# Kernel tuning notes

Measured on AMD Instinct MI355X. Metric: run time of the kernel, lower is better.

The kernel has to match this reference:

```python
import jax, jax.numpy as jnp
import numpy as np

EPS = 1e-05


def setup_inputs() -> dict:
    key = jax.random.key(0)
    k1, k2, k3 = jax.random.split(key, 3)
    b, s, n, m = 16, 4096, 1024, 1024
    x = jax.random.normal(k1, (b, s, n), dtype=jnp.float32)
    # torch.rand -> uniform [0,1)
    A = jax.random.uniform(k2, (m, n), dtype=jnp.float32)
    B = jax.random.uniform(k3, (m, n), dtype=jnp.float32)
    return {"x": x, "A": A, "B": B}


def reference(x, A, B):
    # query: project each token with A, then sum over seq -> [b, m]
    query = jnp.einsum('ij,bsj->bi', A, x)  # fused projection + seq-sum
    query = query / (EPS + jnp.linalg.norm(query, axis=1, keepdims=True))
    # keys: [b, s, m], L2-normalized per token
    keys = jnp.einsum('ij,bsj->bsi', B, x)
    keys = keys / (EPS + jnp.linalg.norm(keys, axis=2, keepdims=True))
    # cosine-style similarity (no softmax): [b, s]
    sim = jnp.einsum('bi,bsi->bs', query, keys)
    # weighted sum of raw inputs: [b, n]
    out = jnp.einsum('bs,bsn->bn', sim, x)
    return (out, sim)
```

## Files before the change

kernel.cpp:

```cpp
#include <hip/hip_runtime.h>

#define EPS 1e-5f

typedef __bf16 bf16x8 __attribute__((ext_vector_type(8)));
typedef __bf16 bf16x4 __attribute__((ext_vector_type(4)));
typedef float f32x4 __attribute__((ext_vector_type(4)));

static __device__ __forceinline__ unsigned int f2bf(float f) {
    unsigned int u = __builtin_bit_cast(unsigned int, f);
    u = (u + 0x7fffu + ((u >> 16) & 1u)) >> 16;
    return u;
}

static __device__ __forceinline__ void gll16(const void* g, void* l) {
    __builtin_amdgcn_global_load_lds(
        (const __attribute__((address_space(1))) unsigned int*)(unsigned long long)g,
        (__attribute__((address_space(3))) unsigned int*)(unsigned int)(unsigned long long)l,
        16, 0, 0);
}

template <int XBF>
__global__ __launch_bounds__(256) void k_prep(const float* __restrict__ x,
                                              float* __restrict__ xs_part,
                                              unsigned short* __restrict__ xbf) {
    const int b = blockIdx.y, sc = blockIdx.x, tid = threadIdx.x;
    const size_t rowbase = ((size_t)(b * 4096 + sc * 128)) * 1024;
    const float4* src = (const float4*)(x + rowbase) + tid;
    uint2* dst = XBF ? ((uint2*)(xbf + rowbase) + tid) : (uint2*)0;
    float ax = 0.f, ay = 0.f, az = 0.f, aw = 0.f;
    for (int r = 0; r < 128; ++r) {
        float4 v = src[r * 256];
        ax += v.x; ay += v.y; az += v.z; aw += v.w;
        if (XBF) {
            uint2 p;
            p.x = f2bf(v.x) | (f2bf(v.y) << 16);
            p.y = f2bf(v.z) | (f2bf(v.w) << 16);
            dst[r * 256] = p;
        }
    }
    float4 o; o.x = ax; o.y = ay; o.z = az; o.w = aw;
    ((float4*)(xs_part + ((size_t)(b * 32 + sc)) * 1024))[tid] = o;
}

__global__ void k_xsred(const float* __restrict__ xs_part, float* __restrict__ xs) {
    const int b = blockIdx.y, j = blockIdx.x * 256 + threadIdx.x;
    const float* p = xs_part + (size_t)b * 32 * 1024 + j;
    float s = 0.f;
#pragma unroll
    for (int sc = 0; sc < 32; ++sc) s += p[sc * 1024];
    xs[b * 1024 + j] = s;
}

__global__ void k_bconv(const float* __restrict__ B, unsigned short* __restrict__ Bb) {
    const int i = blockIdx.x * 256 + threadIdx.x;
    float4 v = ((const float4*)B)[i];
    uint2 p;
    p.x = f2bf(v.x) | (f2bf(v.y) << 16);
    p.y = f2bf(v.z) | (f2bf(v.w) << 16);
    ((uint2*)Bb)[i] = p;
}

__global__ void k_query(const float* __restrict__ A, const float* __restrict__ xs,
                        float* __restrict__ q) {
    const int b = blockIdx.y;
    const int i = blockIdx.x * 256 + threadIdx.x;
    const float4* ar = (const float4*)(A + (size_t)i * 1024);
    const float4* xr = (const float4*)(xs + b * 1024);
    float acc = 0.f;
    for (int k = 0; k < 256; ++k) {
        float4 a = ar[k], v = xr[k];
        acc += a.x * v.x + a.y * v.y + a.z * v.z + a.w * v.w;
    }
    q[b * 1024 + i] = acc;
}

__global__ void k_qnorm(float* q) {
    const int b = blockIdx.x, tid = threadIdx.x;
    float4* qp = (float4*)(q + (size_t)b * 1024);
    float4 v = qp[tid];
    float ss = v.x * v.x + v.y * v.y + v.z * v.z + v.w * v.w;
    for (int o = 1; o < 64; o <<= 1) ss += __shfl_xor(ss, o);
    __shared__ float wsum[4];
    if ((tid & 63) == 0) wsum[tid >> 6] = ss;
    __syncthreads();
    float inv = 1.f / (EPS + sqrtf(wsum[0] + wsum[1] + wsum[2] + wsum[3]));
    v.x *= inv; v.y *= inv; v.z *= inv; v.w *= inv;
    qp[tid] = v;
}

__global__ void k_w(const float* __restrict__ B, const float* __restrict__ q,
                    float* __restrict__ w) {
    const int b = blockIdx.y;
    const int j = blockIdx.x * 256 + threadIdx.x;
    const float* qb = q + (size_t)b * 1024;
    float acc = 0.f;
    for (int i = 0; i < 1024; ++i) acc += B[(size_t)i * 1024 + j] * qb[i];
    w[b * 1024 + j] = acc;
}

__global__ __launch_bounds__(512, 2) void k_nsq8(const unsigned short* __restrict__ xbf,
                                                 const unsigned short* __restrict__ Bb,
                                                 float* __restrict__ nsq_g) {
    __shared__ __align__(16) unsigned short Xs[2][256 * 64];
    __shared__ __align__(16) unsigned short Bs[2][256 * 64];
    __shared__ float nsq_s[256];

    const int tid = threadIdx.x;
    const int lane = tid & 63;
    const int l15 = lane & 15, lg = lane >> 4;
    const int w = tid >> 6;
    const int wm = w >> 2, wn = w & 3;
    const size_t tok0 = (size_t)blockIdx.x * 256;

#define STAGE(s_, buf_)                                                                  \
    do {                                                                                 \
        const int mt_ = (s_) >> 4, ks_ = (s_) & 15;                                      \
        _Pragma("unroll") for (int it = 0; it < 4; ++it) {                               \
            const int g_ = it * 512 + tid;                                               \
            const int row_ = g_ >> 3, c_ = g_ & 7;                                       \
            const int csw_ = (c_ ^ (row_ & 7)) * 8;                                      \
            char* bx_ = (char*)Xs[buf_] + (size_t)(it * 512 + (tid & ~63)) * 16;         \
            gll16(xbf + (tok0 + row_) * 1024 + ks_ * 64 + csw_, bx_);                    \
            char* bb_ = (char*)Bs[buf_] + (size_t)(it * 512 + (tid & ~63)) * 16;         \
            gll16(Bb + (size_t)(mt_ * 256 + row_) * 1024 + ks_ * 64 + csw_, bb_);        \
        }                                                                                \
    } while (0)

    float nsq_reg[8][4];
#pragma unroll
    for (int mi = 0; mi < 8; ++mi)
#pragma unroll
        for (int r = 0; r < 4; ++r) nsq_reg[mi][r] = 0.f;

    f32x4 acc[8][4];

    STAGE(0, 0);
    STAGE(1, 1);

    for (int s = 0; s < 64; ++s) {
        const int buf = s & 1;
        if ((s & 15) == 0) {
#pragma unroll
            for (int mi = 0; mi < 8; ++mi)
#pragma unroll
                for (int ni = 0; ni < 4; ++ni) acc[mi][ni] = (f32x4){0.f, 0.f, 0.f, 0.f};
        }
        if (s < 62) asm volatile("s_waitcnt vmcnt(8)" ::: "memory");
        else        asm volatile("s_waitcnt vmcnt(0)" ::: "memory");
        __builtin_amdgcn_s_barrier();

        const char* xb = (const char*)Xs[buf] + (wm * 128 + l15) * 128;
        const char* bb = (const char*)Bs[buf] + (wn * 64 + l15) * 128;
        const int sw = (l15 & 7) << 4;

        bf16x8 bq[4][2];
#pragma unroll
        for (int ni = 0; ni < 4; ++ni)
#pragma unroll
            for (int kk = 0; kk < 2; ++kk)
                bq[ni][kk] = *(const bf16x8*)(bb + ni * 16 * 128 + ((kk * 64 + lg * 16) ^ sw));

        __builtin_amdgcn_s_setprio(1);
#pragma unroll
        for (int p = 0; p < 4; ++p) {
            bf16x8 a[2][2];
#pragma unroll
            for (int mi = 0; mi < 2; ++mi)
#pragma unroll
                for (int kk = 0; kk < 2; ++kk)
                    a[mi][kk] = *(const bf16x8*)(xb + (p * 2 + mi) * 16 * 128 +
                                                 ((kk * 64 + lg * 16) ^ sw));
#pragma unroll
            for (int mi = 0; mi < 2; ++mi)
#pragma unroll
                for (int ni = 0; ni < 4; ++ni)
#pragma unroll
                    for (int kk = 0; kk < 2; ++kk)
                        acc[p * 2 + mi][ni] = __builtin_amdgcn_mfma_f32_16x16x32_bf16(
                            a[mi][kk], bq[ni][kk], acc[p * 2 + mi][ni], 0, 0, 0);
        }
        __builtin_amdgcn_s_setprio(0);

        asm volatile("" ::: "memory");
        __builtin_amdgcn_s_barrier();
        asm volatile("" ::: "memory");
        if (s + 2 < 64) STAGE(s + 2, buf);

        if ((s & 15) == 15) {
#pragma unroll
            for (int mi = 0; mi < 8; ++mi)
#pragma unroll
                for (int ni = 0; ni < 4; ++ni)
#pragma unroll
                    for (int r = 0; r < 4; ++r)
                        nsq_reg[mi][r] += acc[mi][ni][r] * acc[mi][ni][r];
        }
    }
#undef STAGE

    if (tid < 256) nsq_s[tid] = 0.f;
    __syncthreads();
#pragma unroll
    for (int mi = 0; mi < 8; ++mi)
#pragma unroll
        for (int r = 0; r < 4; ++r) {
            float v = nsq_reg[mi][r];
            v += __shfl_xor(v, 1);
            v += __shfl_xor(v, 2);
            v += __shfl_xor(v, 4);
            v += __shfl_xor(v, 8);
            if (l15 == 0) atomicAdd(&nsq_s[wm * 128 + mi * 16 + lg * 4 + r], v);
        }
    __syncthreads();
    if (tid < 256) nsq_g[tok0 + tid] = nsq_s[tid];
}

__global__ __launch_bounds__(256, 2) void k_nsq_f32(const float* __restrict__ x,
                                                    const unsigned short* __restrict__ Bb,
                                                    float* __restrict__ nsq_g) {
    __shared__ unsigned short Xs[128 * 64];
    __shared__ unsigned short Bs[128 * 64];
    __shared__ float nsq_s[128];

    const int tid = threadIdx.x;
    const int lane = tid & 63;
    const int l15 = lane & 15, lg = lane >> 4;
    const int w = tid >> 6;
    const int wr = w >> 1, wc = w & 1;
    const int st = blockIdx.x * 128;
    const int mh = blockIdx.y;

    float nsq_reg[4][4];
#pragma unroll
    for (int mi = 0; mi < 4; ++mi)
#pragma unroll
        for (int r = 0; r < 4; ++r) nsq_reg[mi][r] = 0.f;

    for (int mti = 0; mti < 4; ++mti) {
        const int mt = mh * 4 + mti;
        f32x4 acc[4][4];
#pragma unroll
        for (int mi = 0; mi < 4; ++mi)
#pragma unroll
            for (int ni = 0; ni < 4; ++ni) acc[mi][ni] = (f32x4){0.f, 0.f, 0.f, 0.f};

        for (int ks = 0; ks < 16; ++ks) {
            __syncthreads();
            {
                const int row = tid >> 1, kh = tid & 1;
                const float* srcx = x + (size_t)(st + row) * 1024 + ks * 64 + kh * 32;
                char* ldsrow = (char*)Xs + row * 128;
                const int sw = (row & 7) << 4;
#pragma unroll
                for (int j = 0; j < 4; ++j) {
                    float4 v0 = ((const float4*)srcx)[j * 2];
                    float4 v1 = ((const float4*)srcx)[j * 2 + 1];
                    uint4 p;
                    p.x = f2bf(v0.x) | (f2bf(v0.y) << 16);
                    p.y = f2bf(v0.z) | (f2bf(v0.w) << 16);
                    p.z = f2bf(v1.x) | (f2bf(v1.y) << 16);
                    p.w = f2bf(v1.z) | (f2bf(v1.w) << 16);
                    *(uint4*)(ldsrow + (((kh * 4 + j) * 16) ^ sw)) = p;
                }
#pragma unroll
                for (int it = 0; it < 4; ++it) {
                    const int idx = it * 256 + tid;
                    const int brow = idx >> 3, c = idx & 7;
                    char* baseB = (char*)Bs + (size_t)(it * 256 + (tid & ~63)) * 16;
                    gll16(Bb + (size_t)(mt * 128 + brow) * 1024 + ks * 64 + (c ^ (brow & 7)) * 8,
                          baseB);
                }
            }
            __syncthreads();

            const char* xb = (const char*)Xs + (wr * 64 + l15) * 128;
            const char* bb = (const char*)Bs + (wc * 64 + l15) * 128;
            const int sw = (l15 & 7) << 4;
#pragma unroll
            for (int kk = 0; kk < 2; ++kk) {
                const int ob = (kk * 64 + lg * 16) ^ sw;
                bf16x8 a[4], bq[4];
#pragma unroll
                for (int mi = 0; mi < 4; ++mi) a[mi] = *(const bf16x8*)(xb + mi * 2048 + ob);
#pragma unroll
                for (int ni = 0; ni < 4; ++ni) bq[ni] = *(const bf16x8*)(bb + ni * 2048 + ob);
#pragma unroll
                for (int mi = 0; mi < 4; ++mi)
#pragma unroll
                    for (int ni = 0; ni < 4; ++ni)
                        acc[mi][ni] = __builtin_amdgcn_mfma_f32_16x16x32_bf16(
                            a[mi], bq[ni], acc[mi][ni], 0, 0, 0);
            }
        }
#pragma unroll
        for (int mi = 0; mi < 4; ++mi)
#pragma unroll
            for (int ni = 0; ni < 4; ++ni)
#pragma unroll
                for (int r = 0; r < 4; ++r)
                    nsq_reg[mi][r] += acc[mi][ni][r] * acc[mi][ni][r];
    }

    if (tid < 128) nsq_s[tid] = 0.f;
    __syncthreads();
#pragma unroll
    for (int mi = 0; mi < 4; ++mi)
#pragma unroll
        for (int r = 0; r < 4; ++r) {
            float v = nsq_reg[mi][r];
            v += __shfl_xor(v, 1);
            v += __shfl_xor(v, 2);
            v += __shfl_xor(v, 4);
            v += __shfl_xor(v, 8);
            if (l15 == 0) atomicAdd(&nsq_s[wr * 64 + mi * 16 + lg * 4 + r], v);
        }
    __syncthreads();
    if (tid < 128) nsq_g[(size_t)mh * 65536 + st + tid] = nsq_s[tid];
}

template <int XBF>
__global__ __launch_bounds__(256, 2) void k_finish(
    const float* __restrict__ x, const unsigned short* __restrict__ xbf,
    const float* __restrict__ w, const float* __restrict__ nsq_g,
    float* __restrict__ outp, float* __restrict__ sim_out) {
    __shared__ __align__(16) unsigned short xt[32 * 1024];
    __shared__ float numer[32];
    __shared__ float simv[32];

    const int tid = threadIdx.x;
    const int bs = blockIdx.x;
    const int b = bs >> 7, s0 = (bs & 127) * 32;
    const size_t tok0 = (size_t)b * 4096 + s0;

    if (XBF) {
#pragma unroll
        for (int it = 0; it < 16; ++it) {
            const int idx = it * 256 + tid;
            const int row = idx >> 7, c = idx & 127;
            char* base = (char*)xt + (size_t)(it * 256 + (tid & ~63)) * 16;
            gll16(xbf + (tok0 + row) * 1024 + ((c ^ (row & 7)) * 8), base);
        }
    } else {
        const float4* src = (const float4*)(x + tok0 * 1024) + tid;
        char* lds = (char*)xt;
        for (int r = 0; r < 32; ++r) {
            float4 v = src[r * 256];
            uint2 p;
            p.x = f2bf(v.x) | (f2bf(v.y) << 16);
            p.y = f2bf(v.z) | (f2bf(v.w) << 16);
            *(uint2*)(lds + r * 2048 + ((tid * 8) ^ ((r & 7) << 4))) = p;
        }
    }
    __syncthreads();

    {
        const int t = tid >> 3, kp = tid & 7;
        const float* wb = w + (size_t)b * 1024 + kp * 128;
        const char* pt = (const char*)xt + t * 2048;
        const int sw2 = (t & 7) << 4;
        float acc = 0.f;
#pragma unroll
        for (int j = 0; j < 16; ++j) {
            const int kb = (kp * 128 + j * 8) * 2;
            bf16x8 v = *(const bf16x8*)(pt + (kb ^ sw2));
#pragma unroll
            for (int e = 0; e < 8; ++e) acc += (float)v[e] * wb[j * 8 + e];
        }
        acc += __shfl_xor(acc, 1);
        acc += __shfl_xor(acc, 2);
        acc += __shfl_xor(acc, 4);
        if (kp == 0) numer[t] = acc;
    }
    __syncthreads();

    if (tid < 32) {
        float nt = XBF ? nsq_g[tok0 + tid] : (nsq_g[tok0 + tid] + nsq_g[65536 + tok0 + tid]);
        float s = numer[tid] / (EPS + sqrtf(nt));
        simv[tid] = s;
        sim_out[tok0 + tid] = s;
    }
    __syncthreads();

    {
        const int n0 = tid * 4;
        float a0 = 0.f, a1 = 0.f, a2 = 0.f, a3 = 0.f;
        const char* lds = (const char*)xt;
#pragma unroll 4
        for (int t = 0; t < 32; ++t) {
            int byte = t * 2048 + ((n0 * 2) ^ ((t & 7) << 4));
            bf16x4 v = *(const bf16x4*)(lds + byte);
            float s = simv[t];
            a0 += s * (float)v[0];
            a1 += s * (float)v[1];
            a2 += s * (float)v[2];
            a3 += s * (float)v[3];
        }
        float4 o; o.x = a0; o.y = a1; o.z = a2; o.w = a3;
        ((float4*)(outp + (size_t)bs * 1024))[tid] = o;
    }
}

__global__ void k_outred(const float* __restrict__ outp, float* __restrict__ out) {
    const int b = blockIdx.y, j = blockIdx.x * 256 + threadIdx.x;
    const float* p = outp + (size_t)b * 128 * 1024 + j;
    float s = 0.f;
    for (int t = 0; t < 128; ++t) s += p[t * 1024];
    out[b * 1024 + j] = s;
}

extern "C" void kernel_launch(void* const* d_in, const int* in_sizes, int n_in,
                              void* d_out, int out_size, void* d_ws, size_t ws_size,
                              hipStream_t stream) {
    const float* x = (const float*)d_in[0];
    const float* A = (const float*)d_in[1];
    const float* B = (const float*)d_in[2];
    float* out = (float*)d_out;
    float* sim = out + 16 * 1024;
    float* ws = (float*)d_ws;
    float* xs_part = ws;
    float* xs = ws + 524288;
    float* q = ws + 540672;
    float* wv = ws + 557056;
    float* nsq = ws + 573440;
    float* outp = ws + 704512;
    unsigned short* Bb = (unsigned short*)(ws + 2801664);
    unsigned short* xbf = (unsigned short*)(ws + 3325952);
    const bool xb = ws_size >= (size_t)(3325952 + 33554432) * 4;

    if (xb) k_prep<1><<<dim3(32, 16), 256, 0, stream>>>(x, xs_part, xbf);
    else    k_prep<0><<<dim3(32, 16), 256, 0, stream>>>(x, xs_part, (unsigned short*)0);
    k_bconv<<<1024, 256, 0, stream>>>(B, Bb);
    k_xsred<<<dim3(4, 16), 256, 0, stream>>>(xs_part, xs);
    k_query<<<dim3(4, 16), 256, 0, stream>>>(A, xs, q);
    k_qnorm<<<16, 256, 0, stream>>>(q);
    k_w<<<dim3(4, 16), 256, 0, stream>>>(B, q, wv);
    if (xb) k_nsq8<<<256, 512, 0, stream>>>(xbf, Bb, nsq);
    else    k_nsq_f32<<<dim3(512, 2), 256, 0, stream>>>(x, Bb, nsq);
    if (xb) k_finish<1><<<2048, 256, 0, stream>>>(x, xbf, wv, nsq, outp, sim);
    else    k_finish<0><<<2048, 256, 0, stream>>>(x, xbf, wv, nsq, outp, sim);
    k_outred<<<dim3(4, 16), 256, 0, stream>>>(outp, out);
}
```

Measured before the change: 324.8 us.

## Fuse finish stage into GEMM kernel and merge small query/norm kernels

Merges the xs reduction into the query kernel and the q normalization into the w kernel, which removes launches. The bf16 key-norm GEMM kernel now also computes sim and the partial weighted sums for its 256 tokens. It reloads x tiles into the reused LDS union, so the separate finish kernel and the nsq round-trip through global memory go away. The GEMM prefetch is split into smaller pieces interleaved across the MFMA sub-steps, with a barrier after each, and the norm reduction is done per m-tile using LDS atomics. In exchange it adds more barriers and runs the finish phase serially at low parallelism (256 blocks), which may leave the GPU underused.

```diff
diff --git a/kernel.cpp b/kernel.cpp
--- a/kernel.cpp
+++ b/kernel.cpp
@@ -4,6 +4,7 @@
 
 typedef __bf16 bf16x8 __attribute__((ext_vector_type(8)));
 typedef __bf16 bf16x4 __attribute__((ext_vector_type(4)));
+typedef __bf16 bf16x2 __attribute__((ext_vector_type(2)));
 typedef float f32x4 __attribute__((ext_vector_type(4)));
 
 static __device__ __forceinline__ unsigned int f2bf(float f) {
@@ -42,15 +43,6 @@
     ((float4*)(xs_part + ((size_t)(b * 32 + sc)) * 1024))[tid] = o;
 }
 
-__global__ void k_xsred(const float* __restrict__ xs_part, float* __restrict__ xs) {
-    const int b = blockIdx.y, j = blockIdx.x * 256 + threadIdx.x;
-    const float* p = xs_part + (size_t)b * 32 * 1024 + j;
-    float s = 0.f;
-#pragma unroll
-    for (int sc = 0; sc < 32; ++sc) s += p[sc * 1024];
-    xs[b * 1024 + j] = s;
-}
-
 __global__ void k_bconv(const float* __restrict__ B, unsigned short* __restrict__ Bb) {
     const int i = blockIdx.x * 256 + threadIdx.x;
     float4 v = ((const float4*)B)[i];
@@ -60,82 +52,107 @@
     ((uint2*)Bb)[i] = p;
 }
 
-__global__ void k_query(const float* __restrict__ A, const float* __restrict__ xs,
-                        float* __restrict__ q) {
-    const int b = blockIdx.y;
-    const int i = blockIdx.x * 256 + threadIdx.x;
+__global__ __launch_bounds__(256) void k_queryf(const float* __restrict__ xs_part,
+                                                const float* __restrict__ A,
+                                                float* __restrict__ q) {
+    __shared__ float xsl[1024];
+    const int b = blockIdx.y, g = blockIdx.x, tid = threadIdx.x;
+    {
+        float4 s4 = {0.f, 0.f, 0.f, 0.f};
+        const float4* p = (const float4*)(xs_part + (size_t)b * 32768) + tid;
+        for (int sc = 0; sc < 32; ++sc) {
+            float4 v = p[sc * 256];
+            s4.x += v.x; s4.y += v.y; s4.z += v.z; s4.w += v.w;
+        }
+        ((float4*)xsl)[tid] = s4;
+    }
+    __syncthreads();
+    const int i = g * 256 + tid;
     const float4* ar = (const float4*)(A + (size_t)i * 1024);
-    const float4* xr = (const float4*)(xs + b * 1024);
     float acc = 0.f;
     for (int k = 0; k < 256; ++k) {
-        float4 a = ar[k], v = xr[k];
+        float4 a = ar[k], v = ((const float4*)xsl)[k];
         acc += a.x * v.x + a.y * v.y + a.z * v.z + a.w * v.w;
     }
     q[b * 1024 + i] = acc;
 }
 
-__global__ void k_qnorm(float* q) {
-    const int b = blockIdx.x, tid = threadIdx.x;
-    float4* qp = (float4*)(q + (size_t)b * 1024);
-    float4 v = qp[tid];
+__global__ __launch_bounds__(256) void k_wf(const float* __restrict__ B,
+                                            const float* __restrict__ q,
+                                            float* __restrict__ w) {
+    __shared__ float ql[1024];
+    __shared__ float wsum[4];
+    const int b = blockIdx.y, g = blockIdx.x, tid = threadIdx.x;
+    float4 v = ((const float4*)(q + (size_t)b * 1024))[tid];
     float ss = v.x * v.x + v.y * v.y + v.z * v.z + v.w * v.w;
     for (int o = 1; o < 64; o <<= 1) ss += __shfl_xor(ss, o);
-    __shared__ float wsum[4];
     if ((tid & 63) == 0) wsum[tid >> 6] = ss;
     __syncthreads();
-    float inv = 1.f / (EPS + sqrtf(wsum[0] + wsum[1] + wsum[2] + wsum[3]));
-    v.x *= inv; v.y *= inv; v.z *= inv; v.w *= inv;
-    qp[tid] = v;
-}
-
-__global__ void k_w(const float* __restrict__ B, const float* __restrict__ q,
-                    float* __restrict__ w) {
-    const int b = blockIdx.y;
-    const int j = blockIdx.x * 256 + threadIdx.x;
-    const float* qb = q + (size_t)b * 1024;
+    const float inv = 1.f / (EPS + sqrtf(wsum[0] + wsum[1] + wsum[2] + wsum[3]));
+    float4 n; n.x = v.x * inv; n.y = v.y * inv; n.z = v.z * inv; n.w = v.w * inv;
+    ((float4*)ql)[tid] = n;
+    __syncthreads();
+    const int j = g * 256 + tid;
     float acc = 0.f;
-    for (int i = 0; i < 1024; ++i) acc += B[(size_t)i * 1024 + j] * qb[i];
+    for (int i = 0; i < 1024; ++i) acc += B[(size_t)i * 1024 + j] * ql[i];
     w[b * 1024 + j] = acc;
 }
 
-__global__ __launch_bounds__(512, 2) void k_nsq8(const unsigned short* __restrict__ xbf,
-                                                 const unsigned short* __restrict__ Bb,
-                                                 float* __restrict__ nsq_g) {
-    __shared__ __align__(16) unsigned short Xs[2][256 * 64];
-    __shared__ __align__(16) unsigned short Bs[2][256 * 64];
+__global__ __launch_bounds__(512, 2) void k_main2(const unsigned short* __restrict__ xbf,
+                                                  const unsigned short* __restrict__ Bb,
+                                                  const float* __restrict__ w,
+                                                  float* __restrict__ outp,
+                                                  float* __restrict__ sim_out) {
+    __shared__ __align__(16) union {
+        struct { unsigned short Xs[2][256 * 64]; unsigned short Bs[2][256 * 64]; } g;
+        unsigned short xt[32 * 1024];
+    } S;
     __shared__ float nsq_s[256];
+    __shared__ float wlds[1024];
+    __shared__ float numer_s[32];
+    __shared__ float simv[32];
 
     const int tid = threadIdx.x;
     const int lane = tid & 63;
     const int l15 = lane & 15, lg = lane >> 4;
-    const int w = tid >> 6;
-    const int wm = w >> 2, wn = w & 3;
-    const size_t tok0 = (size_t)blockIdx.x * 256;
-
-#define STAGE(s_, buf_)                                                                  \
-    do {                                                                                 \
-        const int mt_ = (s_) >> 4, ks_ = (s_) & 15;                                      \
-        _Pragma("unroll") for (int it = 0; it < 4; ++it) {                               \
-            const int g_ = it * 512 + tid;                                               \
-            const int row_ = g_ >> 3, c_ = g_ & 7;                                       \
-            const int csw_ = (c_ ^ (row_ & 7)) * 8;                                      \
-            char* bx_ = (char*)Xs[buf_] + (size_t)(it * 512 + (tid & ~63)) * 16;         \
-            gll16(xbf + (tok0 + row_) * 1024 + ks_ * 64 + csw_, bx_);                    \
-            char* bb_ = (char*)Bs[buf_] + (size_t)(it * 512 + (tid & ~63)) * 16;         \
-            gll16(Bb + (size_t)(mt_ * 256 + row_) * 1024 + ks_ * 64 + csw_, bb_);        \
-        }                                                                                \
+    const int w8 = tid >> 6;
+    const int wm = w8 >> 2, wn = w8 & 3;
+    const int bx = blockIdx.x;
+    const size_t tok0 = (size_t)bx * 256;
+    const int b = bx >> 4;
+
+    ((float2*)wlds)[tid] = ((const float2*)(w + (size_t)b * 1024))[tid];
+    if (tid < 256) nsq_s[tid] = 0.f;
+
+#define STAGE_B(ts_, bf_, it_)                                                            \
+    do {                                                                                  \
+        const int mt_ = (ts_) >> 4, ks_ = (ts_) & 15;                                     \
+        const int g_ = (it_) * 512 + tid;                                                 \
+        const int row_ = g_ >> 3, c_ = g_ & 7;                                            \
+        gll16(Bb + (size_t)(mt_ * 256 + row_) * 1024 + ks_ * 64 + ((c_ ^ (row_ & 7)) * 8),\
+              (char*)S.g.Bs[bf_] + (size_t)((it_) * 512 + (tid & ~63)) * 16);             \
     } while (0)
-
-    float nsq_reg[8][4];
-#pragma unroll
-    for (int mi = 0; mi < 8; ++mi)
-#pragma unroll
-        for (int r = 0; r < 4; ++r) nsq_reg[mi][r] = 0.f;
+#define STAGE_X(ts_, bf_, p_)                                                             \
+    do {                                                                                  \
+        const int ks_ = (ts_) & 15;                                                       \
+        const int w_ = tid >> 6;                                                          \
+        const int ar0_ = (w_ < 4) ? ((p_) * 32 + w_ * 8) : (128 + (p_) * 32 + (w_ - 4) * 8); \
+        const int ar_ = ar0_ + ((tid & 63) >> 3);                                         \
+        const int c_ = tid & 7;                                                           \
+        gll16(xbf + (tok0 + ar_) * 1024 + ks_ * 64 + ((c_ ^ (ar_ & 7)) * 8),              \
+              (char*)S.g.Xs[bf_] + (size_t)ar0_ * 128);                                   \
+    } while (0)
 
     f32x4 acc[8][4];
 
-    STAGE(0, 0);
-    STAGE(1, 1);
+#pragma unroll
+    for (int it = 0; it < 4; ++it) STAGE_B(0, 0, it);
+#pragma unroll
+    for (int pp = 0; pp < 4; ++pp) STAGE_X(0, 0, pp);
+#pragma unroll
+    for (int it = 0; it < 4; ++it) STAGE_B(1, 1, it);
+#pragma unroll
+    for (int pp = 0; pp < 4; ++pp) STAGE_X(1, 1, pp);
 
     for (int s = 0; s < 64; ++s) {
         const int buf = s & 1;
@@ -149,9 +166,10 @@
         else        asm volatile("s_waitcnt vmcnt(0)" ::: "memory");
         __builtin_amdgcn_s_barrier();
 
-        const char* xb = (const char*)Xs[buf] + (wm * 128 + l15) * 128;
-        const char* bb = (const char*)Bs[buf] + (wn * 64 + l15) * 128;
+        const char* xb = (const char*)S.g.Xs[buf] + (wm * 128 + l15) * 128;
+        const char* bb = (const char*)S.g.Bs[buf] + (wn * 64 + l15) * 128;
         const int sw = (l15 & 7) << 4;
+        const bool pre = (s + 2 < 64);
 
         bf16x8 bq[4][2];
 #pragma unroll
@@ -160,7 +178,6 @@
             for (int kk = 0; kk < 2; ++kk)
                 bq[ni][kk] = *(const bf16x8*)(bb + ni * 16 * 128 + ((kk * 64 + lg * 16) ^ sw));
 
-        __builtin_amdgcn_s_setprio(1);
 #pragma unroll
         for (int p = 0; p < 4; ++p) {
             bf16x8 a[2][2];
@@ -170,6 +187,14 @@
                 for (int kk = 0; kk < 2; ++kk)
                     a[mi][kk] = *(const bf16x8*)(xb + (p * 2 + mi) * 16 * 128 +
                                                  ((kk * 64 + lg * 16) ^ sw));
+            if (pre) {
+                if (p == 1) { STAGE_B(s + 2, buf, 0); STAGE_B(s + 2, buf, 1); STAGE_X(s + 2, buf, 0); }
+                if (p == 2) { STAGE_B(s + 2, buf, 2); STAGE_B(s + 2, buf, 3); STAGE_X(s + 2, buf, 1); }
+                if (p == 3) { STAGE_X(s + 2, buf, 2); }
+            }
+            asm volatile("" ::: "memory");
+            __builtin_amdgcn_s_barrier();
+            __builtin_amdgcn_s_setprio(1);
 #pragma unroll
             for (int mi = 0; mi < 2; ++mi)
 #pragma unroll
@@ -178,41 +203,83 @@
                     for (int kk = 0; kk < 2; ++kk)
                         acc[p * 2 + mi][ni] = __builtin_amdgcn_mfma_f32_16x16x32_bf16(
                             a[mi][kk], bq[ni][kk], acc[p * 2 + mi][ni], 0, 0, 0);
-        }
-        __builtin_amdgcn_s_setprio(0);
-
-        asm volatile("" ::: "memory");
-        __builtin_amdgcn_s_barrier();
-        asm volatile("" ::: "memory");
-        if (s + 2 < 64) STAGE(s + 2, buf);
+            __builtin_amdgcn_s_setprio(0);
+            asm volatile("" ::: "memory");
+            __builtin_amdgcn_s_barrier();
+        }
+        if (pre) STAGE_X(s + 2, buf, 3);
 
         if ((s & 15) == 15) {
 #pragma unroll
             for (int mi = 0; mi < 8; ++mi)
 #pragma unroll
-                for (int ni = 0; ni < 4; ++ni)
-#pragma unroll
-                    for (int r = 0; r < 4; ++r)
-                        nsq_reg[mi][r] += acc[mi][ni][r] * acc[mi][ni][r];
-        }
-    }
-#undef STAGE
-
-    if (tid < 256) nsq_s[tid] = 0.f;
-    __syncthreads();
-#pragma unroll
-    for (int mi = 0; mi < 8; ++mi)
-#pragma unroll
-        for (int r = 0; r < 4; ++r) {
-            float v = nsq_reg[mi][r];
-            v += __shfl_xor(v, 1);
-            v += __shfl_xor(v, 2);
-            v += __shfl_xor(v, 4);
-            v += __shfl_xor(v, 8);
-            if (l15 == 0) atomicAdd(&nsq_s[wm * 128 + mi * 16 + lg * 4 + r], v);
-        }
-    __syncthreads();
-    if (tid < 256) nsq_g[tok0 + tid] = nsq_s[tid];
+                for (int r = 0; r < 4; ++r) {
+                    float v = 0.f;
+#pragma unroll
+                    for (int ni = 0; ni < 4; ++ni) v += acc[mi][ni][r] * acc[mi][ni][r];
+                    v += __shfl_xor(v, 1);
+                    v += __shfl_xor(v, 2);
+                    v += __shfl_xor(v, 4);
+                    v += __shfl_xor(v, 8);
+                    if (l15 == 0) atomicAdd(&nsq_s[wm * 128 + mi * 16 + lg * 4 + r], v);
+                }
+        }
+    }
+#undef STAGE_B
+#undef STAGE_X
+    __syncthreads();
+
+    float oa0 = 0.f, oa1 = 0.f;
+    for (int sub = 0; sub < 8; ++sub) {
+#pragma unroll
+        for (int it = 0; it < 8; ++it) {
+            const int idx = it * 512 + tid;
+            const int row = idx >> 7, c = idx & 127;
+            gll16(xbf + (tok0 + sub * 32 + row) * 1024 + (c ^ (row & 7)) * 8,
+                  (char*)S.xt + (size_t)(it * 512 + (tid & ~63)) * 16);
+        }
+        asm volatile("s_waitcnt vmcnt(0)" ::: "memory");
+        __syncthreads();
+        {
+            const int t = tid >> 4, kp = tid & 15;
+            const char* pt = (const char*)S.xt + t * 2048;
+            const int sw2 = (t & 7) << 4;
+            float acc2 = 0.f;
+#pragma unroll
+            for (int j = 0; j < 8; ++j) {
+                bf16x8 v = *(const bf16x8*)(pt + ((j * 256 + kp * 16) ^ sw2));
+                const float* wp = wlds + j * 128 + kp * 8;
+#pragma unroll
+                for (int e = 0; e < 8; ++e) acc2 += (float)v[e] * wp[e];
+            }
+            acc2 += __shfl_xor(acc2, 1);
+            acc2 += __shfl_xor(acc2, 2);
+            acc2 += __shfl_xor(acc2, 4);
+            acc2 += __shfl_xor(acc2, 8);
+            if (kp == 0) numer_s[t] = acc2;
+        }
+        __syncthreads();
+        if (tid < 32) {
+            float sv = numer_s[tid] / (EPS + sqrtf(nsq_s[sub * 32 + tid]));
+            simv[tid] = sv;
+            sim_out[tok0 + sub * 32 + tid] = sv;
+        }
+        __syncthreads();
+        {
+            const char* lds = (const char*)S.xt;
+            const int nb = tid * 4;
+#pragma unroll 4
+            for (int t = 0; t < 32; ++t) {
+                bf16x2 v = *(const bf16x2*)(lds + t * 2048 + (nb ^ ((t & 7) << 4)));
+                float sv = simv[t];
+                oa0 += sv * (float)v[0];
+                oa1 += sv * (float)v[1];
+            }
+        }
+        __syncthreads();
+    }
+    float2 o; o.x = oa0; o.y = oa1;
+    ((float2*)(outp + (size_t)bx * 1024))[tid] = o;
 }
 
 __global__ __launch_bounds__(256, 2) void k_nsq_f32(const float* __restrict__ x,
@@ -318,11 +385,10 @@
     if (tid < 128) nsq_g[(size_t)mh * 65536 + st + tid] = nsq_s[tid];
 }
 
-template <int XBF>
-__global__ __launch_bounds__(256, 2) void k_finish(
-    const float* __restrict__ x, const unsigned short* __restrict__ xbf,
-    const float* __restrict__ w, const float* __restrict__ nsq_g,
-    float* __restrict__ outp, float* __restrict__ sim_out) {
+__global__ __launch_bounds__(256, 2) void k_finish0(
+    const float* __restrict__ x, const float* __restrict__ w,
+    const float* __restrict__ nsq_g, float* __restrict__ outp,
+    float* __restrict__ sim_out) {
     __shared__ __align__(16) unsigned short xt[32 * 1024];
     __shared__ float numer[32];
     __shared__ float simv[32];
@@ -332,24 +398,14 @@
     const int b = bs >> 7, s0 = (bs & 127) * 32;
     const size_t tok0 = (size_t)b * 4096 + s0;
 
-    if (XBF) {
-#pragma unroll
-        for (int it = 0; it < 16; ++it) {
-            const int idx = it * 256 + tid;
-            const int row = idx >> 7, c = idx & 127;
-            char* base = (char*)xt + (size_t)(it * 256 + (tid & ~63)) * 16;
-            gll16(xbf + (tok0 + row) * 1024 + ((c ^ (row & 7)) * 8), base);
-        }
-    } else {
-        const float4* src = (const float4*)(x + tok0 * 1024) + tid;
-        char* lds = (char*)xt;
-        for (int r = 0; r < 32; ++r) {
-            float4 v = src[r * 256];
-            uint2 p;
-            p.x = f2bf(v.x) | (f2bf(v.y) << 16);
-            p.y = f2bf(v.z) | (f2bf(v.w) << 16);
-            *(uint2*)(lds + r * 2048 + ((tid * 8) ^ ((r & 7) << 4))) = p;
-        }
+    const float4* src = (const float4*)(x + tok0 * 1024) + tid;
+    char* lds = (char*)xt;
+    for (int r = 0; r < 32; ++r) {
+        float4 v = src[r * 256];
+        uint2 p;
+        p.x = f2bf(v.x) | (f2bf(v.y) << 16);
+        p.y = f2bf(v.z) | (f2bf(v.w) << 16);
+        *(uint2*)(lds + r * 2048 + ((tid * 8) ^ ((r & 7) << 4))) = p;
     }
     __syncthreads();
 
@@ -374,7 +430,7 @@
     __syncthreads();
 
     if (tid < 32) {
-        float nt = XBF ? nsq_g[tok0 + tid] : (nsq_g[tok0 + tid] + nsq_g[65536 + tok0 + tid]);
+        float nt = nsq_g[tok0 + tid] + nsq_g[65536 + tok0 + tid];
         float s = numer[tid] / (EPS + sqrtf(nt));
         simv[tid] = s;
         sim_out[tok0 + tid] = s;
@@ -384,11 +440,11 @@
     {
         const int n0 = tid * 4;
         float a0 = 0.f, a1 = 0.f, a2 = 0.f, a3 = 0.f;
-        const char* lds = (const char*)xt;
+        const char* p = (const char*)xt;
 #pragma unroll 4
         for (int t = 0; t < 32; ++t) {
             int byte = t * 2048 + ((n0 * 2) ^ ((t & 7) << 4));
-            bf16x4 v = *(const bf16x4*)(lds + byte);
+            bf16x4 v = *(const bf16x4*)(p + byte);
             float s = simv[t];
             a0 += s * (float)v[0];
             a1 += s * (float)v[1];
@@ -400,11 +456,12 @@
     }
 }
 
+template <int NT>
 __global__ void k_outred(const float* __restrict__ outp, float* __restrict__ out) {
     const int b = blockIdx.y, j = blockIdx.x * 256 + threadIdx.x;
-    const float* p = outp + (size_t)b * 128 * 1024 + j;
+    const float* p = outp + (size_t)b * NT * 1024 + j;
     float s = 0.f;
-    for (int t = 0; t < 128; ++t) s += p[t * 1024];
+    for (int t = 0; t < NT; ++t) s += p[t * 1024];
     out[b * 1024 + j] = s;
 }
 
@@ -418,7 +475,6 @@
     float* sim = out + 16 * 1024;
     float* ws = (float*)d_ws;
     float* xs_part = ws;
-    float* xs = ws + 524288;
     float* q = ws + 540672;
     float* wv = ws + 557056;
     float* nsq = ws + 573440;
@@ -430,13 +486,14 @@
     if (xb) k_prep<1><<<dim3(32, 16), 256, 0, stream>>>(x, xs_part, xbf);
     else    k_prep<0><<<dim3(32, 16), 256, 0, stream>>>(x, xs_part, (unsigned short*)0);
     k_bconv<<<1024, 256, 0, stream>>>(B, Bb);
-    k_xsred<<<dim3(4, 16), 256, 0, stream>>>(xs_part, xs);
-    k_query<<<dim3(4, 16), 256, 0, stream>>>(A, xs, q);
-    k_qnorm<<<16, 256, 0, stream>>>(q);
-    k_w<<<dim3(4, 16), 256, 0, stream>>>(B, q, wv);
-    if (xb) k_nsq8<<<256, 512, 0, stream>>>(xbf, Bb, nsq);
-    else    k_nsq_f32<<<dim3(512, 2), 256, 0, stream>>>(x, Bb, nsq);
-    if (xb) k_finish<1><<<2048, 256, 0, stream>>>(x, xbf, wv, nsq, outp, sim);
-    else    k_finish<0><<<2048, 256, 0, stream>>>(x, xbf, wv, nsq, outp, sim);
-    k_outred<<<dim3(4, 16), 256, 0, stream>>>(outp, out);
-}
+    k_queryf<<<dim3(4, 16), 256, 0, stream>>>(xs_part, A, q);
+    k_wf<<<dim3(4, 16), 256, 0, stream>>>(B, q, wv);
+    if (xb) {
+        k_main2<<<256, 512, 0, stream>>>(xbf, Bb, wv, outp, sim);
+        k_outred<16><<<dim3(4, 16), 256, 0, stream>>>(outp, out);
+    } else {
+        k_nsq_f32<<<dim3(512, 2), 256, 0, stream>>>(x, Bb, nsq);
+        k_finish0<<<2048, 256, 0, stream>>>(x, wv, nsq, outp, sim);
+        k_outred<128><<<dim3(4, 16), 256, 0, stream>>>(outp, out);
+    }
+}
```

Measured after the change: 300.7 us. -7.4%, faster.
